# Performance work log

Measured on AMD Instinct MI355X. Metric: run time of the kernel, lower is better.

The kernel has to match this reference:

```python
import jax, jax.numpy as jnp
import numpy as np
import math

EPS = 1e-5
N_HEADS = 4


def _ln(x, g, b):
    mu = jnp.mean(x, axis=-1, keepdims=True)
    var = jnp.mean((x - mu) ** 2, axis=-1, keepdims=True)
    return (x - mu) * jax.lax.rsqrt(var + EPS) * g + b


def _eq_ln(s, v, g, b, vscale):
    # scalar LayerNorm + equivariant vector norm rescaling
    s = _ln(s, g, b)
    vn = jnp.sqrt(jnp.sum(v * v, axis=-1, keepdims=True))  # (B,N,C,1)
    v = v / (vn + EPS) * jnp.mean(vn, axis=-2, keepdims=True) * vscale[None, None, :, None]
    return s, v


def _block(s, v, pos, Wq, bq, Wk, bk, Wv, bv, Wo, bo, w_dist, b_dist, Wvv, Wvo,
           g1, be1, vs1, g2, be2, vs2, Wf1, bf1, Wf2, bf2, Wfv1, Wfv2):
    B, N, S = s.shape
    D = S // N_HEADS
    # --- norm1 + attention ---
    sn, vn = _eq_ln(s, v, g1, be1, vs1)
    q = (sn @ Wq + bq).reshape(B, N, N_HEADS, D)
    k = (sn @ Wk + bk).reshape(B, N, N_HEADS, D)
    vs = (sn @ Wv + bv).reshape(B, N, N_HEADS, D)
    attn = jnp.einsum('bnhd,bmhd->bhnm', q, k) / math.sqrt(D)
    # pairwise Euclidean distance via the |x|^2 + |y|^2 - 2xy trick (clamped for sqrt safety)
    p2 = jnp.sum(pos * pos, axis=-1)  # (B,N)
    d2 = p2[:, :, None] + p2[:, None, :] - 2.0 * jnp.einsum('bnd,bmd->bnm', pos, pos)
    dist = jnp.sqrt(jnp.maximum(d2, 1e-12))  # (B,N,N)
    # dist_proj: Linear(1 -> n_heads) + Softplus, applied per pair
    bias = jax.nn.softplus(dist[..., None] * w_dist + b_dist)  # (B,N,N,H)
    attn = jax.nn.softmax(attn - jnp.transpose(bias, (0, 3, 1, 2)), axis=-1)  # (B,H,N,N)
    attn_mean = jnp.mean(attn, axis=1)  # (B,N,N)
    s_attn = jnp.einsum('bhnm,bmhd->bnhd', attn, vs).reshape(B, N, S) @ Wo + bo
    # vector channel mixing + rotation by head-averaged attention
    v_mix = jnp.einsum('bncx,ce->bnex', vn, Wvv)          # (B,N,C,3)
    v_attn = jnp.einsum('bnm,bmcx->bncx', attn_mean, v_mix)
    v_attn = jnp.einsum('bncx,ce->bnex', v_attn, Wvo)
    s = s + s_attn
    v = v + v_attn
    # --- norm2 + FFN ---
    sn, vn = _eq_ln(s, v, g2, be2, vs2)
    s = s + (jax.nn.gelu(sn @ Wf1 + bf1, approximate=False) @ Wf2 + bf2)
    v = v + jnp.einsum('bnhx,hc->bncx', jnp.einsum('bncx,ch->bnhx', vn, Wfv1), Wfv2)
    return s, v


def setup_inputs() -> dict:
    B, N, S, C, H = 4, 2048, 256, 64, N_HEADS
    key = jax.random.key(0)
    ks = jax.random.split(key, 24)

    def nrm(k, shape, scale=0.02):
        return jax.random.normal(k, shape, dtype=jnp.float32) * scale

    return {
        's': jax.random.normal(ks[0], (B, N, S), dtype=jnp.float32),
        'v': jax.random.normal(ks[1], (B, N, C, 3), dtype=jnp.float32),
        'pos': jax.random.normal(ks[2], (B, N, 3), dtype=jnp.float32),
        'Wq': nrm(ks[3], (S, S)), 'bq': nrm(ks[4], (S,)),
        'Wk': nrm(ks[5], (S, S)), 'bk': nrm(ks[6], (S,)),
        'Wv': nrm(ks[7], (S, S)), 'bv': nrm(ks[8], (S,)),
        'Wo': nrm(ks[9], (S, S)), 'bo': nrm(ks[10], (S,)),
        'w_dist': nrm(ks[11], (H,), 0.5), 'b_dist': nrm(ks[12], (H,), 0.5),
        'Wvv': nrm(ks[13], (C, C)), 'Wvo': nrm(ks[14], (C, C)),
        'g1': jnp.ones((S,), jnp.float32), 'be1': jnp.zeros((S,), jnp.float32),
        'vs1': jnp.ones((C,), jnp.float32),
        'g2': jnp.ones((S,), jnp.float32), 'be2': jnp.zeros((S,), jnp.float32),
        'vs2': jnp.ones((C,), jnp.float32),
        'Wf1': nrm(ks[15], (S, 4 * S)), 'bf1': nrm(ks[16], (4 * S,)),
        'Wf2': nrm(ks[17], (4 * S, S)), 'bf2': nrm(ks[18], (S,)),
        'Wfv1': nrm(ks[19], (C, 4 * C)), 'Wfv2': nrm(ks[20], (4 * C, C)),
    }


def reference(s, v, pos, Wq, bq, Wk, bk, Wv, bv, Wo, bo, w_dist, b_dist, Wvv, Wvo,
              g1, be1, vs1, g2, be2, vs2, Wf1, bf1, Wf2, bf2, Wfv1, Wfv2):
    return _block(s, v, pos, Wq, bq, Wk, bk, Wv, bv, Wo, bo, w_dist, b_dist, Wvv, Wvo,
                  g1, be1, vs1, g2, be2, vs2, Wf1, bf1, Wf2, bf2, Wfv1, Wfv2)
```

## Files before the change

kernel.cpp:

```cpp
#include <hip/hip_runtime.h>
#include <hip/hip_bf16.h>

using bf16 = __hip_bfloat16;
typedef __attribute__((ext_vector_type(8))) short short8;
typedef __attribute__((ext_vector_type(4))) float float4v;
typedef __attribute__((ext_vector_type(16))) float f32x16;
typedef __attribute__((ext_vector_type(4))) unsigned uint4v;

__device__ __forceinline__ float b2f(bf16 x){ return __bfloat162float(x); }
__device__ __forceinline__ bf16  f2b(float x){ return __float2bfloat16(x); }
__device__ __forceinline__ bf16  tob(float x){ return f2b(x); }
__device__ __forceinline__ bf16  tob(bf16 x){ return x; }
__device__ __forceinline__ float frcp(float x){ return __builtin_amdgcn_rcpf(x); }
__device__ __forceinline__ float bs2f(short s){
  unsigned u = ((unsigned)(unsigned short)s) << 16;
  return __builtin_bit_cast(float, u);
}
__device__ __forceinline__ unsigned cvt_pk_bf16(float lo, float hi){
  unsigned r; asm("v_cvt_pk_bf16_f32 %0, %1, %2" : "=v"(r) : "v"(lo), "v"(hi)); return r;
}
__device__ __forceinline__ void plswap(unsigned &a, unsigned &b){
  asm("v_permlane32_swap_b32 %0, %1" : "+v"(a), "+v"(b));
}

#define EPSV 1e-5f
#define Z16 {0.f,0.f,0.f,0.f,0.f,0.f,0.f,0.f,0.f,0.f,0.f,0.f,0.f,0.f,0.f,0.f}

__global__ __launch_bounds__(256) void pos_kernel(const float* __restrict__ pos,
                                                  float* __restrict__ posf, int rows){
  int r = blockIdx.x*256 + threadIdx.x;
  if (r >= rows) return;
  float x = pos[3*r], y = pos[3*r+1], z = pos[3*r+2];
  posf[4*r] = x; posf[4*r+1] = y; posf[4*r+2] = z; posf[4*r+3] = x*x + y*y + z*z;
}

struct WTDesc { const float* src; bf16* dst; int rows, cols; };
struct WTPack { WTDesc d[10]; };

__global__ __launch_bounds__(256) void wtrans_kernel(WTPack p){
  WTDesc w = p.d[blockIdx.z];
  long r0 = (long)blockIdx.y*32, c0 = (long)blockIdx.x*32;
  if (r0 >= w.rows || c0 >= w.cols) return;
  __shared__ bf16 tile[32][33];
  int tx = threadIdx.x & 31, ty = threadIdx.x >> 5;
#pragma unroll
  for (int i = ty; i < 32; i += 8) tile[i][tx] = f2b(w.src[(r0+i)*w.cols + c0 + tx]);
  __syncthreads();
#pragma unroll
  for (int i = ty; i < 32; i += 8) w.dst[(c0+i)*w.rows + r0 + tx] = tile[tx][i];
}

template<typename TI>
__global__ __launch_bounds__(256) void transpose_kernel(
    const TI* __restrict__ in, long ldin, long is1, long is2,
    bf16* __restrict__ out, long ldout, long os1, long os2, int Z2)
{
  int z = blockIdx.z, z1 = z / Z2, z2 = z - z1*Z2;
  in  += (long)z1*is1 + (long)z2*is2;
  out += (long)z1*os1 + (long)z2*os2;
  __shared__ bf16 tile[32][33];
  int tx = threadIdx.x & 31, ty = threadIdx.x >> 5;
  long r0 = (long)blockIdx.y*32, c0 = (long)blockIdx.x*32;
#pragma unroll
  for (int i = ty; i < 32; i += 8) tile[i][tx] = tob(in[(r0+i)*ldin + c0 + tx]);
  __syncthreads();
#pragma unroll
  for (int i = ty; i < 32; i += 8) out[(c0+i)*ldout + r0 + tx] = tile[tx][i];
}

__global__ __launch_bounds__(256) void bcat_kernel(const float* __restrict__ bq,
                                                   const float* __restrict__ bk,
                                                   const float* __restrict__ bv,
                                                   float* __restrict__ bqkv){
  int j = blockIdx.x*256 + threadIdx.x;
  if (j >= 768) return;
  bqkv[j] = (j < 256) ? bq[j] : (j < 512) ? bk[j-256] : bv[j-512];
}

__global__ __launch_bounds__(256) void ln_kernel(const float* __restrict__ x,
                                                 const float* __restrict__ g,
                                                 const float* __restrict__ be,
                                                 bf16* __restrict__ out){
  const long row = blockIdx.x;
  const int t = threadIdx.x;
  __shared__ float r1[256], r2[256];
  float v = x[(row<<8) + t];
  r1[t] = v; r2[t] = v*v; __syncthreads();
  for (int s=128;s>0;s>>=1){
    if (t<s){ r1[t] += r1[t+s]; r2[t] += r2[t+s]; }
    __syncthreads();
  }
  const float mu = r1[0] * (1.f/256.f);
  const float var = r2[0] * (1.f/256.f) - mu*mu;
  const float rstd = rsqrtf(fmaxf(var, 0.f) + EPSV);
  out[(row<<8)+t] = f2b((v-mu)*rstd*g[t] + be[t]);
}

__global__ __launch_bounds__(192) void vnorm1_kernel(const float* __restrict__ vin,
                                                     const float* __restrict__ vs1,
                                                     bf16* __restrict__ vnX){
  const long row = blockIdx.x;
  const int t = threadIdx.x;
  __shared__ float vv[192], nrm[64];
  __shared__ float smean;
  vv[t] = vin[row*192 + t];
  __syncthreads();
  if (t < 64){
    float a = vv[3*t], b = vv[3*t+1], c = vv[3*t+2];
    nrm[t] = sqrtf(a*a + b*b + c*c);
  }
  __syncthreads();
  if (t == 0){ float s = 0.f; for (int i=0;i<64;i++) s += nrm[i]; smean = s*(1.f/64.f); }
  __syncthreads();
  const int c = t/3, x = t - 3*c;
  const float val = vv[t] / (nrm[c] + EPSV) * smean * vs1[c];
  vnX[row*192 + x*64 + c] = f2b(val);
}

__global__ __launch_bounds__(192) void vnorm2_kernel(const float* __restrict__ v2X,
                                                     const float* __restrict__ vs2,
                                                     bf16* __restrict__ vn2X){
  const long row = blockIdx.x;
  const int t = threadIdx.x;
  __shared__ float vv[192], nrm[64];
  __shared__ float smean;
  vv[t] = v2X[row*192 + t];
  __syncthreads();
  if (t < 64){
    float a = vv[t], b = vv[t+64], c = vv[t+128];
    nrm[t] = sqrtf(a*a + b*b + c*c);
  }
  __syncthreads();
  if (t == 0){ float s = 0.f; for (int i=0;i<64;i++) s += nrm[i]; smean = s*(1.f/64.f); }
  __syncthreads();
  const int c = t & 63;
  vn2X[row*192 + t] = f2b(vv[t] / (nrm[c] + EPSV) * smean * vs2[c]);
}

__global__ __launch_bounds__(256) void knorm_kernel(const bf16* __restrict__ qkv,
                                                    float* __restrict__ kmax){
  const int bh = blockIdx.x, b = bh>>2, h = bh&3;
  const int t = threadIdx.x;
  __shared__ float red[256];
  float mx = 0.f;
  for (int r=0;r<8;r++){
    long row = (long)b*2048 + r*256 + t;
    const short8* kp = (const short8*)(qkv + row*768 + 256 + h*64);
    float ss = 0.f;
#pragma unroll
    for (int c=0;c<8;c++){
      short8 v = kp[c];
#pragma unroll
      for (int j=0;j<8;j++){ float f = bs2f(v[j]); ss = fmaf(f,f,ss); }
    }
    mx = fmaxf(mx, ss);
  }
  red[t] = mx; __syncthreads();
  for (int s=128;s>0;s>>=1){ if (t<s) red[t] = fmaxf(red[t], red[t+s]); __syncthreads(); }
  if (t==0) kmax[bh] = sqrtf(red[0]);
}

#define ATT_K_OFF   0
#define ATT_V_OFF   4096
#define ATT_X_OFF   9216
#define ATT_P_OFF   24576
#define ATT_TILE    25088
#define ATT_GRP     50176
#define ATT_LACC    98304
#define ATT_SMEM    100352

__global__ __launch_bounds__(512, 2) void attn_kernel(
    const bf16* __restrict__ qkv,
    const bf16* __restrict__ vsT,
    const bf16* __restrict__ vmixT,
    const float* __restrict__ posf,
    const float* __restrict__ kmaxA,
    const float* __restrict__ w_dist, const float* __restrict__ b_dist,
    bf16* __restrict__ sA,
    bf16* __restrict__ slab)
{
  __shared__ __align__(16) char smem[ATT_SMEM];
  const int qb = blockIdx.x;
  const int bh = blockIdx.y;
  const int b  = bh >> 2, h = bh & 3;
  const int tid = threadIdx.x;
  const int w = tid >> 6, lane = tid & 63;
  const int g = w >> 2, qw = w & 3;
  const int lq = lane & 31, hi = lane >> 5;
  const int gtid = tid & 255;

  const int qloc = qb*128 + qw*32 + lq;
  const long rowQ = (long)b*2048 + qloc;

  short8 qf[4];
  {
    const bf16* qp = qkv + rowQ*768 + h*64 + hi*8;
#pragma unroll
    for (int kc=0;kc<4;kc++) qf[kc] = *(const short8*)(qp + kc*16);
  }
  float q2 = 0.f;
#pragma unroll
  for (int kc=0;kc<4;kc++)
#pragma unroll
    for (int j=0;j<8;j++){ float qv = bs2f(qf[kc][j]); q2 = fmaf(qv,qv,q2); }
  q2 += __shfl_xor(q2, 32);
  const float mxs = sqrtf(q2) * kmaxA[bh] * 0.125f;
  const float wh = w_dist[h], bhd = b_dist[h];
  const float4v pn = *(const float4v*)(posf + (long)b*8192 + (long)qloc*4);
  const float m2x = -2.f*pn[0], m2y = -2.f*pn[1], m2z = -2.f*pn[2], pnw = pn[3];

  f32x16 O[2]  = {Z16, Z16};
  f32x16 VM[6] = {Z16, Z16, Z16, Z16, Z16, Z16};
  float lacc = 0.f;

  short8 stK, stV, stX0, stX1, stX2; float4v stP;
  const int sm = gtid >> 3, sc = gtid & 7;
  const int vd = gtid >> 2, vc = gtid & 3;
  const bf16* Kg = qkv + (long)b*2048*768 + 256 + h*64;
  const bf16* Vg = vsT + (long)b*524288 + (long)h*131072;
  const bf16* Xg = vmixT + (long)b*393216;
  const float* Pg = posf + (long)b*8192;
  char* gbase = smem + g*ATT_GRP;

  auto LOADT = [&](int m0){
    stK  = *(const short8*)(Kg + (long)(m0+sm)*768 + sc*8);
    stV  = *(const short8*)(Vg + (long)vd*2048 + m0 + vc*8);
    stX0 = *(const short8*)(Xg + (long)vd*2048 + m0 + vc*8);
    stX1 = *(const short8*)(Xg + (long)(64+vd)*2048 + m0 + vc*8);
    stX2 = *(const short8*)(Xg + (long)(128+vd)*2048 + m0 + vc*8);
    if (gtid < 32) stP = *(const float4v*)(Pg + (long)(m0+gtid)*4);
  };
  auto WRITET = [&](char* buf){
    *(short8*)(buf + ATT_K_OFF + sm*128 + ((sc ^ (sm&7))<<4)) = stK;
    *(short8*)(buf + ATT_V_OFF + vd*80 + vc*16) = stV;
    *(short8*)(buf + ATT_X_OFF + vd*80 + vc*16) = stX0;
    *(short8*)(buf + ATT_X_OFF + (64+vd)*80 + vc*16) = stX1;
    *(short8*)(buf + ATT_X_OFF + (128+vd)*80 + vc*16) = stX2;
    if (gtid < 32) *(float4v*)(buf + ATT_P_OFF + gtid*16) = stP;
  };

  auto COMPUTE = [&](const char* buf){
    const char* Kb = buf + ATT_K_OFF;
    const char* Vb = buf + ATT_V_OFF;
    const char* Xb = buf + ATT_X_OFF;
    const float4v* pmb = (const float4v*)(buf + ATT_P_OFF);
    f32x16 S = Z16;
#pragma unroll
    for (int kc=0;kc<4;kc++){
      short8 kf = *(const short8*)(Kb + lq*128 + (((kc*2+hi) ^ (lq&7))<<4));
      S = __builtin_amdgcn_mfma_f32_32x32x16_bf16(kf, qf[kc], S, 0, 0, 0);
    }
    float P[16];
#pragma unroll
    for (int gg=0; gg<4; gg++){
#pragma unroll
      for (int i=0;i<4;i++){
        float4v pm = pmb[gg*8 + hi*4 + i];
        float d2 = fmaf(m2x, pm[0], fmaf(m2y, pm[1], fmaf(m2z, pm[2], pnw + pm[3])));
        float dist = sqrtf(fmaxf(d2, 1e-12f));
        float sig = frcp(1.f + __expf(fmaf(dist, wh, bhd)));
        float p = __expf(fmaf(S[gg*4+i], 0.125f, -mxs)) * sig;
        lacc += p;
        P[gg*4+i] = p;
      }
    }
    unsigned pk[8];
#pragma unroll
    for (int t=0;t<8;t++) pk[t] = cvt_pk_bf16(P[2*t], P[2*t+1]);
    plswap(pk[0], pk[2]); plswap(pk[1], pk[3]);
    plswap(pk[4], pk[6]); plswap(pk[5], pk[7]);
    uint4v y0v = {pk[0], pk[1], pk[2], pk[3]};
    uint4v y1v = {pk[4], pk[5], pk[6], pk[7]};
    short8 Y0 = __builtin_bit_cast(short8, y0v);
    short8 Y1 = __builtin_bit_cast(short8, y1v);
#pragma unroll
    for (int dblk=0; dblk<2; dblk++){
      short8 v0 = *(const short8*)(Vb + (dblk*32+lq)*80 + hi*16);
      short8 v1 = *(const short8*)(Vb + (dblk*32+lq)*80 + 32 + hi*16);
      O[dblk] = __builtin_amdgcn_mfma_f32_32x32x16_bf16(v0, Y0, O[dblk], 0,0,0);
      O[dblk] = __builtin_amdgcn_mfma_f32_32x32x16_bf16(v1, Y1, O[dblk], 0,0,0);
    }
#pragma unroll
    for (int eblk=0; eblk<6; eblk++){
      short8 x0 = *(const short8*)(Xb + (eblk*32+lq)*80 + hi*16);
      short8 x1 = *(const short8*)(Xb + (eblk*32+lq)*80 + 32 + hi*16);
      VM[eblk] = __builtin_amdgcn_mfma_f32_32x32x16_bf16(x0, Y0, VM[eblk], 0,0,0);
      VM[eblk] = __builtin_amdgcn_mfma_f32_32x32x16_bf16(x1, Y1, VM[eblk], 0,0,0);
    }
  };

  LOADT(g*32);
  WRITET(gbase);
  __syncthreads();
#pragma unroll 1
  for (int i=0; i<32; ++i){
    if (i < 31) LOADT((2*(i+1)+g)*32);
    COMPUTE(gbase + (i&1)*ATT_TILE);
    if (i < 31) WRITET(gbase + ((i+1)&1)*ATT_TILE);
    __syncthreads();
  }

  float* laccT = (float*)(smem + ATT_LACC);
  laccT[w*64 + lane] = lacc;
  if (g == 1){
    float* Od = (float*)(smem + ATT_GRP) + (qw*64+lane)*33;
#pragma unroll
    for (int r=0;r<16;r++){ Od[r] = O[0][r]; Od[16+r] = O[1][r]; }
  }
  __syncthreads();
  const float lsum = laccT[qw*64+lq] + laccT[qw*64+32+lq]
                   + laccT[(4+qw)*64+lq] + laccT[(4+qw)*64+32+lq];
  if (g == 0){
    const float* Od = (const float*)(smem + ATT_GRP) + (qw*64+lane)*33;
#pragma unroll
    for (int r=0;r<16;r++){ O[0][r] += Od[r]; O[1][r] += Od[16+r]; }
  }
  __syncthreads();
#pragma unroll
  for (int hf=0; hf<2; hf++){
    if (g == 0){
      float* Vd = (float*)smem + (qw*64+lane)*49;
#pragma unroll
      for (int e=0;e<3;e++)
#pragma unroll
        for (int r=0;r<16;r++) Vd[e*16+r] = VM[hf*3+e][r];
    }
    __syncthreads();
    if (g == 1){
      const float* Vd = (const float*)smem + (qw*64+lane)*49;
#pragma unroll
      for (int e=0;e<3;e++)
#pragma unroll
        for (int r=0;r<16;r++) VM[hf*3+e][r] += Vd[e*16+r];
    }
    __syncthreads();
  }

  const float sinv = frcp(lsum);
  if (g == 0){
    char* scr = smem + qw*12544;
#pragma unroll
    for (int dblk=0; dblk<2; dblk++)
#pragma unroll
      for (int pp=0; pp<8; pp++){
        const int r = 2*pp;
        const int d = dblk*32 + (r&3) + 8*(r>>2) + 4*hi;
        unsigned u = cvt_pk_bf16(O[dblk][r]*sinv, O[dblk][r+1]*sinv);
        *(unsigned*)(scr + lq*136 + d*2) = u;
      }
  } else {
    const float vinv = 0.25f * sinv;
    char* scr = smem + ATT_GRP + qw*12544;
#pragma unroll
    for (int eblk=0; eblk<6; eblk++)
#pragma unroll
      for (int pp=0; pp<8; pp++){
        const int r = 2*pp;
        const int e = eblk*32 + (r&3) + 8*(r>>2) + 4*hi;
        unsigned u = cvt_pk_bf16(VM[eblk][r]*vinv, VM[eblk][r+1]*vinv);
        *(unsigned*)(scr + lq*392 + e*2) = u;
      }
  }
  __syncthreads();
  if (g == 0){
    const char* scr = smem + qw*12544;
    const int q = lane >> 1, half = lane & 1;
    const char* src = scr + q*136 + half*64;
    char* dst = (char*)(sA + (long)(b*2048 + qb*128 + qw*32 + q)*256 + h*64 + half*32);
#pragma unroll
    for (int i=0;i<8;i++)
      *(unsigned long long*)(dst + i*8) = *(const unsigned long long*)(src + i*8);
  } else {
    const char* scr = smem + ATT_GRP + qw*12544;
    const int q = lane >> 1, half = lane & 1;
    const char* src = scr + q*392 + half*192;
    char* dst = (char*)(slab + (long)h*1572864
                        + (long)(b*2048 + qb*128 + qw*32 + q)*192 + half*96);
#pragma unroll
    for (int i=0;i<24;i++)
      *(unsigned long long*)(dst + i*8) = *(const unsigned long long*)(src + i*8);
  }
}

__global__ __launch_bounds__(256) void hred_kernel(const bf16* __restrict__ slab,
                                                   bf16* __restrict__ out){
  long i = (long)blockIdx.x*256 + threadIdx.x;
  if (i >= 196608) return;
  const short8* s0 = (const short8*)slab + i;
  short8 a = s0[0], b = s0[196608], c = s0[2*196608], d = s0[3*196608];
  short8 o;
#pragma unroll
  for (int j=0;j<8;j++){
    float f = bs2f(a[j]) + bs2f(b[j]) + bs2f(c[j]) + bs2f(d[j]);
    bf16 hv = f2b(f); o[j] = *(short*)&hv;
  }
  ((short8*)out)[i] = o;
}

template<int MT, int NT, int ACT, int OUTM, int RXIL, int CXIL, int SWZ>
__global__ __launch_bounds__(64) void gemm_kernel(
    const bf16* __restrict__ A, long lda, long As1, long As2,
    const bf16* __restrict__ BT, long ldb, long Bs1, long Bs2,
    const float* __restrict__ bias,
    const float* __restrict__ resid, long ldr, long Rs1, long Rs2,
    void* __restrict__ Cv, long ldc, long Cs1, long Cs2,
    int K, int Z2, int KS)
{
  int z = blockIdx.z;
  int zz = z / KS, ks = z - zz*KS;
  int z1 = zz / Z2, z2 = zz - z1*Z2;
  A  += (long)z1*As1 + (long)z2*As2 + (long)ks*K;
  BT += (long)z1*Bs1 + (long)z2*Bs2 + (long)ks*K;
  if (resid) resid += (long)z1*Rs1 + (long)z2*Rs2;
  const long cbase = (long)z1*Cs1 + (long)z2*Cs2;

  int bx = blockIdx.x, by = blockIdx.y;
  if (SWZ){
    const int nx = gridDim.x, ny = gridDim.y;
    long lin = (long)by*nx + bx;
    const int xcd = (int)(lin & 7);
    long idx = lin >> 3;
    const int rpx = ny >> 3;
    by = xcd*rpx + (int)(idx / nx);
    bx = (int)(idx % nx);
  }

  const int lane = threadIdx.x;
  const int col = lane & 15, quad = lane >> 4;
  const long rowA0 = (long)by*(16*MT);
  const long colB0 = (long)bx*(16*NT);

  float4v acc[MT][NT];
#pragma unroll
  for (int m=0;m<MT;m++)
#pragma unroll
    for (int n=0;n<NT;n++) acc[m][n] = (float4v){0.f,0.f,0.f,0.f};

  const bf16* ap[MT];
  const bf16* bp[NT];
#pragma unroll
  for (int m=0;m<MT;m++) ap[m] = A + (rowA0 + m*16 + col)*lda + quad*8;
#pragma unroll
  for (int n=0;n<NT;n++) bp[n] = BT + (colB0 + n*16 + col)*ldb + quad*8;

  for (int k0 = 0; k0 < K; k0 += 32){
    short8 a[MT], bb[NT];
#pragma unroll
    for (int m=0;m<MT;m++){ a[m] = *(const short8*)ap[m]; ap[m] += 32; }
#pragma unroll
    for (int n=0;n<NT;n++){ bb[n] = *(const short8*)bp[n]; bp[n] += 32; }
#pragma unroll
    for (int m=0;m<MT;m++)
#pragma unroll
      for (int n=0;n<NT;n++)
        acc[m][n] = __builtin_amdgcn_mfma_f32_16x16x32_bf16(a[m], bb[n], acc[m][n], 0, 0, 0);
  }

#pragma unroll
  for (int m=0;m<MT;m++){
    const long ri = rowA0 + m*16 + quad*4;
#pragma unroll
    for (int n=0;n<NT;n++){
      const long cj = colB0 + n*16 + col;
      const float bbias = bias ? bias[cj] : 0.f;
#pragma unroll
      for (int r=0;r<4;r++){
        const long ci = ri + r;
        float val = acc[m][n][r] + bbias;
        if (ACT == 1) val = 0.5f*val*(1.f + erff(val*0.70710678118654752f));
        if (resid){
          const long raddr = RXIL ? ((ci/3)*192 + cj*3 + (ci%3)) : (ci*ldr + cj);
          val += resid[raddr];
        }
        const long caddr = CXIL ? (cbase + (ci/3)*192 + cj*3 + (ci%3))
                                : (cbase + ci*ldc + cj);
        if (OUTM == 0)      ((bf16*)Cv)[caddr] = f2b(val);
        else if (OUTM == 1) ((float*)Cv)[caddr] = val;
        else                unsafeAtomicAdd(&((float*)Cv)[caddr], val);
      }
    }
  }
}

extern "C" void kernel_launch(void* const* d_in, const int* in_sizes, int n_in,
                              void* d_out, int out_size, void* d_ws, size_t ws_size,
                              hipStream_t stream)
{
  const float* s    = (const float*)d_in[0];
  const float* v    = (const float*)d_in[1];
  const float* pos  = (const float*)d_in[2];
  const float* Wq   = (const float*)d_in[3];
  const float* bq   = (const float*)d_in[4];
  const float* Wk   = (const float*)d_in[5];
  const float* bk   = (const float*)d_in[6];
  const float* Wv   = (const float*)d_in[7];
  const float* bv   = (const float*)d_in[8];
  const float* Wo   = (const float*)d_in[9];
  const float* bo   = (const float*)d_in[10];
  const float* w_d  = (const float*)d_in[11];
  const float* b_d  = (const float*)d_in[12];
  const float* Wvv  = (const float*)d_in[13];
  const float* Wvo  = (const float*)d_in[14];
  const float* g1   = (const float*)d_in[15];
  const float* be1  = (const float*)d_in[16];
  const float* vs1  = (const float*)d_in[17];
  const float* g2   = (const float*)d_in[18];
  const float* be2  = (const float*)d_in[19];
  const float* vs2  = (const float*)d_in[20];
  const float* Wf1  = (const float*)d_in[21];
  const float* bf1  = (const float*)d_in[22];
  const float* Wf2  = (const float*)d_in[23];
  const float* bf2  = (const float*)d_in[24];
  const float* Wfv1 = (const float*)d_in[25];
  const float* Wfv2 = (const float*)d_in[26];

  float* outS = (float*)d_out;
  float* outV = outS + (size_t)4*2048*256;

  char* w = (char*)d_ws;
  size_t o = 0;
  auto alloc = [&](size_t bytes)->char* {
    char* p = w + o;
    o = (o + bytes + 255) & ~(size_t)255;
    return p;
  };
  float* posf  = (float*)alloc(131072);
  bf16* WqkvT = (bf16*)alloc(393216);
  bf16* WoT   = (bf16*)alloc(131072);
  bf16* Wf1T  = (bf16*)alloc(524288);
  bf16* Wf2T  = (bf16*)alloc(524288);
  bf16* WvvT  = (bf16*)alloc(8192);
  bf16* WvoT  = (bf16*)alloc(8192);
  bf16* Wfv1T = (bf16*)alloc(32768);
  bf16* Wfv2T = (bf16*)alloc(32768);
  float* bqkv = (float*)alloc(3072);
  float* kmax = (float*)alloc(64);
  bf16* sn    = (bf16*)alloc(4194304);
  bf16* qkv   = (bf16*)alloc(12582912);
  bf16* vsT   = (bf16*)alloc(4194304);
  bf16* sA    = (bf16*)alloc(4194304);
  float* s2   = (float*)alloc(8388608);
  bf16* vnX   = (bf16*)alloc(3145728);
  bf16* vmixX = (bf16*)alloc(3145728);
  bf16* vmixXT= (bf16*)alloc(3145728);
  float* v2X  = (float*)alloc(6291456);
  bf16* slab  = (bf16*)alloc(12582912);
  bf16* h1    = (bf16*)alloc(16777216);
  bf16* vn2X  = vnX;
  bf16* tvXb  = vmixX;
  bf16* hv    = qkv;
  if (o > ws_size) return;

  pos_kernel<<<32, 256, 0, stream>>>(pos, posf, 8192);
  WTPack pk;
  pk.d[0] = {Wq,   WqkvT,          256, 256};
  pk.d[1] = {Wk,   WqkvT + 65536,  256, 256};
  pk.d[2] = {Wv,   WqkvT + 131072, 256, 256};
  pk.d[3] = {Wo,   WoT,            256, 256};
  pk.d[4] = {Wf1,  Wf1T,           256, 1024};
  pk.d[5] = {Wf2,  Wf2T,           1024, 256};
  pk.d[6] = {Wvv,  WvvT,           64, 64};
  pk.d[7] = {Wvo,  WvoT,           64, 64};
  pk.d[8] = {Wfv1, Wfv1T,          64, 256};
  pk.d[9] = {Wfv2, Wfv2T,          256, 64};
  wtrans_kernel<<<dim3(32,32,10), 256, 0, stream>>>(pk);
  bcat_kernel<<<3, 256, 0, stream>>>(bq, bk, bv, bqkv);

  ln_kernel<<<8192, 256, 0, stream>>>(s, g1, be1, sn);
  vnorm1_kernel<<<8192, 192, 0, stream>>>(v, vs1, vnX);

  gemm_kernel<2,4,0,0,0,0,0><<<dim3(1,768,1), 64, 0, stream>>>(vnX,64,0,0, WvvT,64,0,0,
      nullptr, nullptr,0,0,0, vmixX,64,0,0, 64, 1, 1);
  transpose_kernel<bf16><<<dim3(6,64,4), 256, 0, stream>>>(vmixX, 192, 393216,0,
      vmixXT, 2048, 393216,0, 1);

  gemm_kernel<2,4,0,0,0,0,1><<<dim3(12,256,1), 64, 0, stream>>>(sn,256,0,0, WqkvT,256,0,0,
      bqkv, nullptr,0,0,0, qkv,768,0,0, 256, 1, 1);
  transpose_kernel<bf16><<<dim3(2,64,16), 256, 0, stream>>>(qkv+512, 768, 1572864,64,
      vsT, 2048, 524288,131072, 4);

  knorm_kernel<<<16, 256, 0, stream>>>(qkv, kmax);
  attn_kernel<<<dim3(16,16), 512, 0, stream>>>(qkv, vsT, vmixXT, posf, kmax,
      w_d, b_d, sA, slab);
  hred_kernel<<<768, 256, 0, stream>>>(slab, tvXb);

  gemm_kernel<2,4,0,1,0,0,1><<<dim3(4,256,1), 64, 0, stream>>>(sA,256,0,0, WoT,256,0,0,
      bo, s,256,0,0, s2,256,0,0, 256, 1, 1);

  gemm_kernel<2,4,0,1,1,0,0><<<dim3(1,768,1), 64, 0, stream>>>(tvXb,64,0,0, WvoT,64,0,0,
      nullptr, v,0,0,0, v2X,64,0,0, 64, 1, 1);

  ln_kernel<<<8192, 256, 0, stream>>>(s2, g2, be2, sn);
  gemm_kernel<2,4,1,0,0,0,1><<<dim3(16,256,1), 64, 0, stream>>>(sn,256,0,0, Wf1T,256,0,0,
      bf1, nullptr,0,0,0, h1,1024,0,0, 256, 1, 1);
  gemm_kernel<2,4,0,1,0,0,1><<<dim3(4,256,1), 64, 0, stream>>>(h1,1024,0,0, Wf2T,1024,0,0,
      bf2, s2,256,0,0, outS,256,0,0, 1024, 1, 1);

  vnorm2_kernel<<<8192, 192, 0, stream>>>(v2X, vs2, vn2X);
  gemm_kernel<2,4,0,0,0,0,1><<<dim3(4,768,1), 64, 0, stream>>>(vn2X,64,0,0, Wfv1T,64,0,0,
      nullptr, nullptr,0,0,0, hv,256,0,0, 64, 1, 1);
  gemm_kernel<2,4,0,1,0,1,0><<<dim3(1,768,1), 64, 0, stream>>>(hv,256,0,0, Wfv2T,256,0,0,
      nullptr, v2X,64,0,0, outV,0,0,0, 256, 1, 1);
}
```

Before: 425.9 us.

## Add LDS-tiled 128x128 GEMM for large projections and split key-norm reduction

```diff
diff --git a/kernel.cpp b/kernel.cpp
--- a/kernel.cpp
+++ b/kernel.cpp
@@ -71,8 +71,10 @@
 __global__ __launch_bounds__(256) void bcat_kernel(const float* __restrict__ bq,
                                                    const float* __restrict__ bk,
                                                    const float* __restrict__ bv,
-                                                   float* __restrict__ bqkv){
+                                                   float* __restrict__ bqkv,
+                                                   float* __restrict__ kmax){
   int j = blockIdx.x*256 + threadIdx.x;
+  if (blockIdx.x == 0 && threadIdx.x < 16) kmax[threadIdx.x] = 0.f;
   if (j >= 768) return;
   bqkv[j] = (j < 256) ? bq[j] : (j < 512) ? bk[j-256] : bv[j-512];
 }
@@ -142,22 +144,18 @@
   const int bh = blockIdx.x, b = bh>>2, h = bh&3;
   const int t = threadIdx.x;
   __shared__ float red[256];
-  float mx = 0.f;
-  for (int r=0;r<8;r++){
-    long row = (long)b*2048 + r*256 + t;
-    const short8* kp = (const short8*)(qkv + row*768 + 256 + h*64);
-    float ss = 0.f;
-#pragma unroll
-    for (int c=0;c<8;c++){
-      short8 v = kp[c];
-#pragma unroll
-      for (int j=0;j<8;j++){ float f = bs2f(v[j]); ss = fmaf(f,f,ss); }
-    }
-    mx = fmaxf(mx, ss);
-  }
-  red[t] = mx; __syncthreads();
+  long row = (long)b*2048 + (long)blockIdx.y*256 + t;
+  const short8* kp = (const short8*)(qkv + row*768 + 256 + h*64);
+  float ss = 0.f;
+#pragma unroll
+  for (int c=0;c<8;c++){
+    short8 v = kp[c];
+#pragma unroll
+    for (int j=0;j<8;j++){ float f = bs2f(v[j]); ss = fmaf(f,f,ss); }
+  }
+  red[t] = ss; __syncthreads();
   for (int s=128;s>0;s>>=1){ if (t<s) red[t] = fmaxf(red[t], red[t+s]); __syncthreads(); }
-  if (t==0) kmax[bh] = sqrtf(red[0]);
+  if (t==0) atomicMax((unsigned*)&kmax[bh], __float_as_uint(red[0]));
 }
 
 #define ATT_K_OFF   0
@@ -204,7 +202,7 @@
 #pragma unroll
     for (int j=0;j<8;j++){ float qv = bs2f(qf[kc][j]); q2 = fmaf(qv,qv,q2); }
   q2 += __shfl_xor(q2, 32);
-  const float mxs = sqrtf(q2) * kmaxA[bh] * 0.125f;
+  const float mxs = sqrtf(q2 * kmaxA[bh]) * 0.125f;
   const float wh = w_dist[h], bhd = b_dist[h];
   const float4v pn = *(const float4v*)(posf + (long)b*8192 + (long)qloc*4);
   const float m2x = -2.f*pn[0], m2y = -2.f*pn[1], m2z = -2.f*pn[2], pnw = pn[3];
@@ -397,7 +395,93 @@
   ((short8*)out)[i] = o;
 }
 
-template<int MT, int NT, int ACT, int OUTM, int RXIL, int CXIL, int SWZ>
+template<int ACT, int OUTM>
+__global__ __launch_bounds__(256) void tgemm_kernel(
+    const bf16* __restrict__ A, long lda,
+    const bf16* __restrict__ BT, long ldb,
+    const float* __restrict__ bias,
+    const float* __restrict__ resid,
+    void* __restrict__ Cv, long ldc,
+    int K)
+{
+  __shared__ __align__(16) bf16 As[2][128*32];
+  __shared__ __align__(16) bf16 Bs[2][128*32];
+  const int tid = threadIdx.x;
+  const int w = tid >> 6, lane = tid & 63;
+  const int wr = w >> 1, wc = w & 1;
+  const int col = lane & 15, quad = lane >> 4;
+  const long rowA0 = (long)blockIdx.y*128;
+  const long colB0 = (long)blockIdx.x*128;
+
+  const int tr = tid >> 2, tc = tid & 3;
+  const bf16* Ag = A + (rowA0 + tr)*lda + tc*8;
+  const bf16* Bg = BT + (colB0 + tr)*ldb + tc*8;
+
+  short8 sa[2], sb[2];
+  auto LOAD = [&](int k0){
+#pragma unroll
+    for (int c=0;c<2;c++){
+      sa[c] = *(const short8*)(Ag + (long)c*64*lda + k0);
+      sb[c] = *(const short8*)(Bg + (long)c*64*ldb + k0);
+    }
+  };
+  auto STORE = [&](int buf){
+#pragma unroll
+    for (int c=0;c<2;c++){
+      *(short8*)(&As[buf][(tr + 64*c)*32 + tc*8]) = sa[c];
+      *(short8*)(&Bs[buf][(tr + 64*c)*32 + tc*8]) = sb[c];
+    }
+  };
+
+  float4v acc[4][4];
+#pragma unroll
+  for (int m=0;m<4;m++)
+#pragma unroll
+    for (int n=0;n<4;n++) acc[m][n] = (float4v){0.f,0.f,0.f,0.f};
+
+  LOAD(0); STORE(0);
+  __syncthreads();
+  const int nk = K >> 5;
+#pragma unroll 1
+  for (int ks=0; ks<nk; ++ks){
+    if (ks+1 < nk) LOAD((ks+1)*32);
+    const bf16* Ab = &As[ks&1][(wr*64 + col)*32 + quad*8];
+    const bf16* Bb = &Bs[ks&1][(wc*64 + col)*32 + quad*8];
+    short8 af[4], bfv[4];
+#pragma unroll
+    for (int m=0;m<4;m++) af[m] = *(const short8*)(Ab + m*16*32);
+#pragma unroll
+    for (int n=0;n<4;n++) bfv[n] = *(const short8*)(Bb + n*16*32);
+#pragma unroll
+    for (int m=0;m<4;m++)
+#pragma unroll
+      for (int n=0;n<4;n++)
+        acc[m][n] = __builtin_amdgcn_mfma_f32_16x16x32_bf16(af[m], bfv[n], acc[m][n], 0, 0, 0);
+    if (ks+1 < nk) STORE((ks+1)&1);
+    __syncthreads();
+  }
+
+#pragma unroll
+  for (int m=0;m<4;m++){
+    const long ci0 = rowA0 + wr*64 + m*16 + quad*4;
+#pragma unroll
+    for (int n=0;n<4;n++){
+      const long cj = colB0 + wc*64 + n*16 + col;
+      const float bbias = bias ? bias[cj] : 0.f;
+#pragma unroll
+      for (int r=0;r<4;r++){
+        const long ci = ci0 + r;
+        float val = acc[m][n][r] + bbias;
+        if (ACT == 1) val = 0.5f*val*(1.f + erff(val*0.70710678118654752f));
+        if (resid) val += resid[ci*ldc + cj];
+        if (OUTM == 0) ((bf16*)Cv)[ci*ldc + cj] = f2b(val);
+        else           ((float*)Cv)[ci*ldc + cj] = val;
+      }
+    }
+  }
+}
+
+template<int MT, int NT, int ACT, int OUTM, int RXIL, int CXIL>
 __global__ __launch_bounds__(64) void gemm_kernel(
     const bf16* __restrict__ A, long lda, long As1, long As2,
     const bf16* __restrict__ BT, long ldb, long Bs1, long Bs2,
@@ -414,21 +498,10 @@
   if (resid) resid += (long)z1*Rs1 + (long)z2*Rs2;
   const long cbase = (long)z1*Cs1 + (long)z2*Cs2;
 
-  int bx = blockIdx.x, by = blockIdx.y;
-  if (SWZ){
-    const int nx = gridDim.x, ny = gridDim.y;
-    long lin = (long)by*nx + bx;
-    const int xcd = (int)(lin & 7);
-    long idx = lin >> 3;
-    const int rpx = ny >> 3;
-    by = xcd*rpx + (int)(idx / nx);
-    bx = (int)(idx % nx);
-  }
-
   const int lane = threadIdx.x;
   const int col = lane & 15, quad = lane >> 4;
-  const long rowA0 = (long)by*(16*MT);
-  const long colB0 = (long)bx*(16*NT);
+  const long rowA0 = (long)blockIdx.y*(16*MT);
+  const long colB0 = (long)blockIdx.x*(16*NT);
 
   float4v acc[MT][NT];
 #pragma unroll
@@ -564,41 +637,41 @@
   pk.d[8] = {Wfv1, Wfv1T,          64, 256};
   pk.d[9] = {Wfv2, Wfv2T,          256, 64};
   wtrans_kernel<<<dim3(32,32,10), 256, 0, stream>>>(pk);
-  bcat_kernel<<<3, 256, 0, stream>>>(bq, bk, bv, bqkv);
+  bcat_kernel<<<3, 256, 0, stream>>>(bq, bk, bv, bqkv, kmax);
 
   ln_kernel<<<8192, 256, 0, stream>>>(s, g1, be1, sn);
   vnorm1_kernel<<<8192, 192, 0, stream>>>(v, vs1, vnX);
 
-  gemm_kernel<2,4,0,0,0,0,0><<<dim3(1,768,1), 64, 0, stream>>>(vnX,64,0,0, WvvT,64,0,0,
+  gemm_kernel<2,4,0,0,0,0><<<dim3(1,768,1), 64, 0, stream>>>(vnX,64,0,0, WvvT,64,0,0,
       nullptr, nullptr,0,0,0, vmixX,64,0,0, 64, 1, 1);
   transpose_kernel<bf16><<<dim3(6,64,4), 256, 0, stream>>>(vmixX, 192, 393216,0,
       vmixXT, 2048, 393216,0, 1);
 
-  gemm_kernel<2,4,0,0,0,0,1><<<dim3(12,256,1), 64, 0, stream>>>(sn,256,0,0, WqkvT,256,0,0,
-      bqkv, nullptr,0,0,0, qkv,768,0,0, 256, 1, 1);
+  tgemm_kernel<0,0><<<dim3(6,64), 256, 0, stream>>>(sn,256, WqkvT,256,
+      bqkv, nullptr, qkv,768, 256);
   transpose_kernel<bf16><<<dim3(2,64,16), 256, 0, stream>>>(qkv+512, 768, 1572864,64,
       vsT, 2048, 524288,131072, 4);
 
-  knorm_kernel<<<16, 256, 0, stream>>>(qkv, kmax);
+  knorm_kernel<<<dim3(16,8), 256, 0, stream>>>(qkv, kmax);
   attn_kernel<<<dim3(16,16), 512, 0, stream>>>(qkv, vsT, vmixXT, posf, kmax,
       w_d, b_d, sA, slab);
   hred_kernel<<<768, 256, 0, stream>>>(slab, tvXb);
 
-  gemm_kernel<2,4,0,1,0,0,1><<<dim3(4,256,1), 64, 0, stream>>>(sA,256,0,0, WoT,256,0,0,
-      bo, s,256,0,0, s2,256,0,0, 256, 1, 1);
-
-  gemm_kernel<2,4,0,1,1,0,0><<<dim3(1,768,1), 64, 0, stream>>>(tvXb,64,0,0, WvoT,64,0,0,
+  tgemm_kernel<0,1><<<dim3(2,64), 256, 0, stream>>>(sA,256, WoT,256,
+      bo, s, s2,256, 256);
+
+  gemm_kernel<2,4,0,1,1,0><<<dim3(1,768,1), 64, 0, stream>>>(tvXb,64,0,0, WvoT,64,0,0,
       nullptr, v,0,0,0, v2X,64,0,0, 64, 1, 1);
 
   ln_kernel<<<8192, 256, 0, stream>>>(s2, g2, be2, sn);
-  gemm_kernel<2,4,1,0,0,0,1><<<dim3(16,256,1), 64, 0, stream>>>(sn,256,0,0, Wf1T,256,0,0,
-      bf1, nullptr,0,0,0, h1,1024,0,0, 256, 1, 1);
-  gemm_kernel<2,4,0,1,0,0,1><<<dim3(4,256,1), 64, 0, stream>>>(h1,1024,0,0, Wf2T,1024,0,0,
-      bf2, s2,256,0,0, outS,256,0,0, 1024, 1, 1);
+  tgemm_kernel<1,0><<<dim3(8,64), 256, 0, stream>>>(sn,256, Wf1T,256,
+      bf1, nullptr, h1,1024, 256);
+  tgemm_kernel<0,1><<<dim3(2,64), 256, 0, stream>>>(h1,1024, Wf2T,1024,
+      bf2, s2, outS,256, 1024);
 
   vnorm2_kernel<<<8192, 192, 0, stream>>>(v2X, vs2, vn2X);
-  gemm_kernel<2,4,0,0,0,0,1><<<dim3(4,768,1), 64, 0, stream>>>(vn2X,64,0,0, Wfv1T,64,0,0,
+  gemm_kernel<2,4,0,0,0,0><<<dim3(4,768,1), 64, 0, stream>>>(vn2X,64,0,0, Wfv1T,64,0,0,
       nullptr, nullptr,0,0,0, hv,256,0,0, 64, 1, 1);
-  gemm_kernel<2,4,0,1,0,1,0><<<dim3(1,768,1), 64, 0, stream>>>(hv,256,0,0, Wfv2T,256,0,0,
+  gemm_kernel<2,4,0,1,0,1><<<dim3(1,768,1), 64, 0, stream>>>(hv,256,0,0, Wfv2T,256,0,0,
       nullptr, v2X,64,0,0, outV,0,0,0, 256, 1, 1);
 }
```

Result: faster. 403.2 us (-5.3%).
